# Optimization experiments

Measured on AMD Instinct MI355X. Metric: run time of the kernel, lower is better.

Reference implementation:

```python
import jax, jax.numpy as jnp
import numpy as np

B, S, D = 4, 2048, 2048
H, DH = 16, 128


def setup_inputs() -> dict:
    key = jax.random.key(0)
    k1, k2, k3, k4, k5 = jax.random.split(key, 5)
    x = jax.random.normal(k1, (B, S, D), dtype=jnp.float32)
    # causal mask, broadcast over heads and batch (module does mask.unsqueeze(0))
    attn_mask = jnp.tril(jnp.ones((S, S), dtype=jnp.int32))
    # torch Linear weights: [out, in]; scaled like default init
    w_qkv = jax.random.normal(k2, (3 * H * DH, D), dtype=jnp.float32) / np.sqrt(D)
    b_qkv = jax.random.normal(k3, (3 * H * DH,), dtype=jnp.float32) * 0.01
    w_out = jax.random.normal(k4, (D, H * DH), dtype=jnp.float32) / np.sqrt(H * DH)
    b_out = jax.random.normal(k5, (D,), dtype=jnp.float32) * 0.01
    return {"x": x, "attn_mask": attn_mask, "w_qkv": w_qkv, "b_qkv": b_qkv,
            "w_out": w_out, "b_out": b_out}


def reference(x, attn_mask, w_qkv, b_qkv, w_out, b_out):
    b, s, d = x.shape
    qkv = x @ w_qkv.T + b_qkv                      # [B,S,3*H*DH]
    qkv = qkv.reshape(b, s, H, 3 * DH)             # per-head contiguous 3*DH slice
    qkv = jnp.transpose(qkv, (2, 0, 1, 3))         # [H,B,S,3*DH]
    q, k, v = jnp.split(qkv, 3, axis=-1)           # each [H,B,S,DH]
    scores = jnp.einsum('hbqd,hbkd->hbqk', q, k) / np.sqrt(DH)
    scores = jnp.where(attn_mask[None, None] == 0, -jnp.inf, scores)
    attn = jax.nn.softmax(scores, axis=-1)         # dropout is identity at eval
    ctx = jnp.einsum('hbqk,hbkd->hbqd', attn, v)   # [H,B,S,DH]
    ctx = jnp.transpose(ctx, (1, 2, 0, 3)).reshape(b, s, H * DH)
    return ctx @ w_out.T + b_out
```

## Files before the change

### kernel.cpp

```cpp
#include <hip/hip_runtime.h>

typedef unsigned short u16;
typedef __bf16 bf16x8 __attribute__((ext_vector_type(8)));
typedef unsigned short u16x8 __attribute__((ext_vector_type(8)));
typedef float f32x4 __attribute__((ext_vector_type(4)));

#define GLDS16(gp, lp)                                                        \
  __builtin_amdgcn_global_load_lds(                                           \
      (const __attribute__((address_space(1))) void*)(gp),                    \
      (__attribute__((address_space(3))) void*)(lp), 16, 0, 0)

__device__ __forceinline__ u16 f2bf(float f) {
  unsigned u = __float_as_uint(f);
  u += 0x7FFFu + ((u >> 16) & 1u);
  return (u16)(u >> 16);
}

__device__ __forceinline__ f32x4 mfma_bf16(bf16x8 a, bf16x8 b, f32x4 c) {
  return __builtin_amdgcn_mfma_f32_16x16x32_bf16(a, b, c, 0, 0, 0);
}

__global__ void cvt_f32_bf16(const float* __restrict__ src,
                             u16* __restrict__ dst, int n8) {
  for (int i = blockIdx.x * blockDim.x + threadIdx.x; i < n8;
       i += gridDim.x * blockDim.x) {
    const float4* sp = (const float4*)src + (size_t)i * 2;
    float4 a = sp[0], b = sp[1];
    u16x8 o;
    o[0] = f2bf(a.x); o[1] = f2bf(a.y); o[2] = f2bf(a.z); o[3] = f2bf(a.w);
    o[4] = f2bf(b.x); o[5] = f2bf(b.y); o[6] = f2bf(b.z); o[7] = f2bf(b.w);
    *((u16x8*)dst + i) = o;
  }
}

template <int OUT_BF16>
__global__ __launch_bounds__(256) void gemm_bt(const u16* __restrict__ A,
                                               const u16* __restrict__ B,
                                               const float* __restrict__ bias,
                                               void* __restrict__ Cout, int M,
                                               int N, int K) {
  __shared__ __attribute__((aligned(16))) u16 As[128 * 64];
  __shared__ __attribute__((aligned(16))) u16 Bs[128 * 64];
  const int t = threadIdx.x, lane = t & 63, w = t >> 6;
  const int l15 = lane & 15, l4 = lane >> 4;
  const int bm = blockIdx.x * 128, bn = blockIdx.y * 128;
  const int wr = (w >> 1) * 64, wc = (w & 1) * 64;

  f32x4 z4 = {0.f, 0.f, 0.f, 0.f};
  f32x4 acc[4][4];
#pragma unroll
  for (int i = 0; i < 4; ++i)
#pragma unroll
    for (int j = 0; j < 4; ++j) acc[i][j] = z4;

  const int srow = t >> 3;
  const int scol = ((t & 7) ^ (srow & 7)) << 3;
  const u16* Ag = A + (size_t)(bm + srow) * K + scol;
  const u16* Bg = B + (size_t)(bn + srow) * K + scol;
  u16* AsW = As + w * 512;
  u16* BsW = Bs + w * 512;

  for (int k0 = 0; k0 < K; k0 += 64) {
    __syncthreads();
#pragma unroll
    for (int i = 0; i < 4; ++i) {
      GLDS16(Ag + k0 + i * 32 * K, AsW + i * 2048);
      GLDS16(Bg + k0 + i * 32 * K, BsW + i * 2048);
    }
    __syncthreads();
#pragma unroll
    for (int kc = 0; kc < 2; ++kc) {
      bf16x8 af[4], bf[4];
#pragma unroll
      for (int x = 0; x < 4; ++x) {
        int ra = wr + x * 16 + l15;
        af[x] = *(const bf16x8*)(As + ra * 64 + (((kc * 4 + l4) ^ (ra & 7)) << 3));
        int rb = wc + x * 16 + l15;
        bf[x] = *(const bf16x8*)(Bs + rb * 64 + (((kc * 4 + l4) ^ (rb & 7)) << 3));
      }
#pragma unroll
      for (int mi = 0; mi < 4; ++mi)
#pragma unroll
        for (int ni = 0; ni < 4; ++ni)
          acc[mi][ni] = mfma_bf16(af[mi], bf[ni], acc[mi][ni]);
    }
  }
  const int cr = l4 * 4, cc = l15;
#pragma unroll
  for (int ni = 0; ni < 4; ++ni) {
    int col = bn + wc + ni * 16 + cc;
    float bv = bias[col];
#pragma unroll
    for (int mi = 0; mi < 4; ++mi)
#pragma unroll
      for (int r = 0; r < 4; ++r) {
        int row = bm + wr + mi * 16 + cr + r;
        float v = acc[mi][ni][r] + bv;
        if (OUT_BF16)
          ((u16*)Cout)[(size_t)row * N + col] = f2bf(v);
        else
          ((float*)Cout)[(size_t)row * N + col] = v;
      }
  }
}

__device__ __forceinline__ int vt_idx(int d, int kk) {
  int swz = (d ^ (d >> 3)) & 7;
  return d * 64 + ((((kk >> 3) ^ swz) << 3) | (kk & 7));
}
__device__ __forceinline__ int ps_idx(int r, int c) {
  return r * 64 + ((((c >> 3) ^ ((r >> 2) & 7)) << 3) | (c & 7));
}

__global__ __launch_bounds__(256) void attn_fwd(const u16* __restrict__ qkv,
                                                u16* __restrict__ ctx) {
  constexpr int NQ = 6144, SD = 2048;
  __shared__ __attribute__((aligned(16))) u16 Ks[2][64 * 128];
  __shared__ __attribute__((aligned(16))) u16 Vt[2][128 * 64];
  __shared__ __attribute__((aligned(16))) u16 Ps[64 * 64];
  const int t = threadIdx.x, lane = t & 63, w = t >> 6;
  const int l15 = lane & 15, l4 = lane >> 4;
  const int h = blockIdx.y, b = blockIdx.z;
  const size_t rowbase = (size_t)b * SD;
  const int hq = h * 384;

  const u16* Kg = qkv + (rowbase + (t >> 4)) * NQ + hq + 128 +
                  (((t & 15) ^ ((t >> 4) & 7)) << 3);
  const u16* Vg = qkv + (rowbase + (t & 15)) * NQ + hq + 256 + ((t >> 4) << 3);
  const int vkk = t & 15, vd0 = (t >> 4) << 3;

  const float C = 0.12751879522447905f;
  const float THRC = 62.73592239488341f;

  for (int seg = 0; seg < 2; ++seg) {
    const int q0 = (seg == 0 ? (31 - (int)blockIdx.x) : (int)blockIdx.x) * 64;
    const int nt = (q0 >> 6) + 1;
    const int qrow = q0 + w * 16 + l4 * 4;

    bf16x8 qf[4];
    {
      const u16* qp = qkv + (rowbase + q0 + w * 16 + l15) * NQ + hq + l4 * 8;
#pragma unroll
      for (int kc = 0; kc < 4; ++kc) qf[kc] = *(const bf16x8*)(qp + kc * 32);
    }

    f32x4 z4 = {0.f, 0.f, 0.f, 0.f};
    f32x4 oacc[8];
#pragma unroll
    for (int i = 0; i < 8; ++i) oacc[i] = z4;
    float m_run[4], l_run[4];
#pragma unroll
    for (int r = 0; r < 4; ++r) { m_run[r] = -3.0e38f; l_run[r] = 0.f; }

    u16x8 vA[4], vB[4];
#pragma unroll
    for (int i = 0; i < 4; ++i)
      GLDS16(Kg + (size_t)(i * 16) * NQ, &Ks[0][i * 2048 + w * 512]);
#pragma unroll
    for (int p = 0; p < 4; ++p)
      vA[p] = *(const u16x8*)(Vg + (size_t)(p * 16) * NQ);
    __syncthreads();
#pragma unroll
    for (int p = 0; p < 4; ++p) {
      int kk = p * 16 + vkk;
#pragma unroll
      for (int j = 0; j < 8; ++j) Vt[0][vt_idx(vd0 + j, kk)] = vA[p][j];
    }
    {
      const int kv = (nt > 1) ? 64 : 0;
#pragma unroll
      for (int p = 0; p < 4; ++p)
        vA[p] = *(const u16x8*)(Vg + (size_t)(kv + p * 16) * NQ);
    }
    __syncthreads();

    for (int tt = 0; tt < nt; ++tt) {
      const int k0 = tt * 64, cur = tt & 1;
      const u16* KsC = &Ks[cur][0];
      u16* KsN = &Ks[cur ^ 1][0];
      const u16* VtC = &Vt[cur][0];
      u16* VtN = &Vt[cur ^ 1][0];

      const int kn = (k0 + 64 <= q0) ? k0 + 64 : q0;
#pragma unroll
      for (int i = 0; i < 4; ++i)
        GLDS16(Kg + (size_t)(kn + i * 16) * NQ, KsN + i * 2048 + w * 512);
      const int kv = (k0 + 128 <= q0) ? k0 + 128 : q0;
#pragma unroll
      for (int p = 0; p < 4; ++p)
        vB[p] = *(const u16x8*)(Vg + (size_t)(kv + p * 16) * NQ);

      f32x4 sc[4];
#pragma unroll
      for (int nf = 0; nf < 4; ++nf) sc[nf] = z4;
#pragma unroll
      for (int kc = 0; kc < 4; ++kc)
#pragma unroll
        for (int nf = 0; nf < 4; ++nf) {
          int rk = nf * 16 + l15;
          bf16x8 kf = *(const bf16x8*)(KsC + rk * 128 +
                                       (((kc * 4 + l4) ^ (rk & 7)) << 3));
          sc[nf] = mfma_bf16(qf[kc], kf, sc[nf]);
        }
      if (k0 == q0) {
#pragma unroll
        for (int nf = 0; nf < 4; ++nf) {
          int col = k0 + nf * 16 + l15;
#pragma unroll
          for (int r = 0; r < 4; ++r)
            if (col > qrow + r) sc[nf][r] = -3.0e38f;
        }
      }
      float mx[4];
#pragma unroll
      for (int r = 0; r < 4; ++r)
        mx[r] = fmaxf(fmaxf(sc[0][r], sc[1][r]), fmaxf(sc[2][r], sc[3][r]));
#pragma unroll
      for (int off = 8; off >= 1; off >>= 1)
#pragma unroll
        for (int r = 0; r < 4; ++r)
          mx[r] = fmaxf(mx[r], __shfl_xor(mx[r], off));
      bool upd = false;
#pragma unroll
      for (int r = 0; r < 4; ++r) upd |= (mx[r] > m_run[r] + THRC);
      if (__any(upd)) {
#pragma unroll
        for (int r = 0; r < 4; ++r) {
          float mn = fmaxf(m_run[r], mx[r]);
          float cr = exp2f((m_run[r] - mn) * C);
          m_run[r] = mn;
          l_run[r] *= cr;
#pragma unroll
          for (int nf = 0; nf < 8; ++nf) oacc[nf][r] *= cr;
        }
      }
      float mC[4], sm[4];
#pragma unroll
      for (int r = 0; r < 4; ++r) mC[r] = m_run[r] * C;
#pragma unroll
      for (int nf = 0; nf < 4; ++nf)
#pragma unroll
        for (int r = 0; r < 4; ++r)
          sc[nf][r] = exp2f(fmaf(sc[nf][r], C, -mC[r]));
#pragma unroll
      for (int r = 0; r < 4; ++r)
        sm[r] = (sc[0][r] + sc[1][r]) + (sc[2][r] + sc[3][r]);
#pragma unroll
      for (int off = 8; off >= 1; off >>= 1)
#pragma unroll
        for (int r = 0; r < 4; ++r) sm[r] += __shfl_xor(sm[r], off);
#pragma unroll
      for (int r = 0; r < 4; ++r) l_run[r] += sm[r];
#pragma unroll
      for (int nf = 0; nf < 4; ++nf)
#pragma unroll
        for (int r = 0; r < 4; ++r)
          ((__bf16*)Ps)[ps_idx(w * 16 + l4 * 4 + r, nf * 16 + l15)] =
              (__bf16)sc[nf][r];
#pragma unroll
      for (int p = 0; p < 4; ++p) {
        int kk = p * 16 + vkk;
#pragma unroll
        for (int j = 0; j < 8; ++j) VtN[vt_idx(vd0 + j, kk)] = vA[p][j];
      }
#pragma unroll
      for (int kc = 0; kc < 2; ++kc) {
        bf16x8 pf =
            *(const bf16x8*)(Ps + ps_idx(w * 16 + l15, kc * 32 + l4 * 8));
#pragma unroll
        for (int nf = 0; nf < 8; ++nf) {
          bf16x8 vf =
              *(const bf16x8*)(VtC + vt_idx(nf * 16 + l15, kc * 32 + l4 * 8));
          oacc[nf] = mfma_bf16(pf, vf, oacc[nf]);
        }
      }
      __syncthreads();
#pragma unroll
      for (int p = 0; p < 4; ++p) vA[p] = vB[p];
    }
    float inv[4];
#pragma unroll
    for (int r = 0; r < 4; ++r) inv[r] = 1.f / l_run[r];
    u16* cp = ctx + (rowbase + q0 + w * 16 + l4 * 4) * SD + h * 128 + l15;
#pragma unroll
    for (int nf = 0; nf < 8; ++nf)
#pragma unroll
      for (int r = 0; r < 4; ++r)
        ((__bf16*)cp)[(size_t)r * SD + nf * 16] =
            (__bf16)(oacc[nf][r] * inv[r]);
  }
}

extern "C" void kernel_launch(void* const* d_in, const int* in_sizes, int n_in,
                              void* d_out, int out_size, void* d_ws,
                              size_t ws_size, hipStream_t stream) {
  const float* x = (const float*)d_in[0];
  const float* wqkv = (const float*)d_in[2];
  const float* bqkv = (const float*)d_in[3];
  const float* wout = (const float*)d_in[4];
  const float* bout = (const float*)d_in[5];
  float* out = (float*)d_out;
  char* ws = (char*)d_ws;

  u16* xb = (u16*)(ws);
  u16* wqkvb = (u16*)(ws + 33554432);
  u16* woutb = (u16*)(ws + 58720256);
  u16* qkvb = (u16*)(ws + 67108864);
  u16* ctx = xb;

  cvt_f32_bf16<<<2048, 256, 0, stream>>>(x, xb, 16777216 / 8);
  cvt_f32_bf16<<<2048, 256, 0, stream>>>(wqkv, wqkvb, 12582912 / 8);
  cvt_f32_bf16<<<1024, 256, 0, stream>>>(wout, woutb, 4194304 / 8);
  gemm_bt<1><<<dim3(64, 48), 256, 0, stream>>>(xb, wqkvb, bqkv, qkvb, 8192,
                                               6144, 2048);
  attn_fwd<<<dim3(16, 16, 4), 256, 0, stream>>>(qkvb, ctx);
  gemm_bt<0><<<dim3(64, 16), 256, 0, stream>>>(ctx, woutb, bout, out, 8192,
                                               2048, 2048);
}
```

Before: 705.5 us.

## Enlarge attention query tile to 128 rows so each K/V tile is reused twice

The attention kernel now handles 128 query rows per block, two 16-row fragments per wave, instead of 64. Each K and V tile loaded into LDS therefore feeds twice as many MFMAs, which halves K/V global and LDS traffic per unit of work. The grid shrinks from 16 to 8 query-tile pairs and launch bounds request 2 blocks per CU. In exchange the kernel needs more accumulator registers and a larger Ps buffer, and the reduced block count may lower occupancy and worsen load balance.

```diff
diff --git a/kernel.cpp b/kernel.cpp
--- a/kernel.cpp
+++ b/kernel.cpp
@@ -112,16 +112,16 @@
   return r * 64 + ((((c >> 3) ^ ((r >> 2) & 7)) << 3) | (c & 7));
 }
 
-__global__ __launch_bounds__(256) void attn_fwd(const u16* __restrict__ qkv,
-                                                u16* __restrict__ ctx) {
+__global__ __launch_bounds__(256, 2) void attn_fwd(const u16* __restrict__ qkv,
+                                                   u16* __restrict__ ctx) {
   constexpr int NQ = 6144, SD = 2048;
   __shared__ __attribute__((aligned(16))) u16 Ks[2][64 * 128];
   __shared__ __attribute__((aligned(16))) u16 Vt[2][128 * 64];
-  __shared__ __attribute__((aligned(16))) u16 Ps[64 * 64];
+  __shared__ __attribute__((aligned(16))) u16 Ps[128 * 64];
   const int t = threadIdx.x, lane = t & 63, w = t >> 6;
   const int l15 = lane & 15, l4 = lane >> 4;
   const int h = blockIdx.y, b = blockIdx.z;
-  const size_t rowbase = (size_t)b * SD;
+  const size_t rowbase = (size_t)b * 2048;
   const int hq = h * 384;
 
   const u16* Kg = qkv + (rowbase + (t >> 4)) * NQ + hq + 128 +
@@ -133,24 +133,31 @@
   const float THRC = 62.73592239488341f;
 
   for (int seg = 0; seg < 2; ++seg) {
-    const int q0 = (seg == 0 ? (31 - (int)blockIdx.x) : (int)blockIdx.x) * 64;
-    const int nt = (q0 >> 6) + 1;
-    const int qrow = q0 + w * 16 + l4 * 4;
-
-    bf16x8 qf[4];
-    {
-      const u16* qp = qkv + (rowbase + q0 + w * 16 + l15) * NQ + hq + l4 * 8;
-#pragma unroll
-      for (int kc = 0; kc < 4; ++kc) qf[kc] = *(const bf16x8*)(qp + kc * 32);
+    const int qt = (seg == 0) ? (15 - (int)blockIdx.x) : (int)blockIdx.x;
+    const int q0 = qt * 128;
+    const int nt = 2 * qt + 2;
+    const int qr0 = q0 + w * 32 + l4 * 4;
+
+    bf16x8 qf[2][4];
+#pragma unroll
+    for (int mi = 0; mi < 2; ++mi) {
+      const u16* qp =
+          qkv + (rowbase + q0 + w * 32 + mi * 16 + l15) * NQ + hq + l4 * 8;
+#pragma unroll
+      for (int kc = 0; kc < 4; ++kc) qf[mi][kc] = *(const bf16x8*)(qp + kc * 32);
     }
 
     f32x4 z4 = {0.f, 0.f, 0.f, 0.f};
-    f32x4 oacc[8];
-#pragma unroll
-    for (int i = 0; i < 8; ++i) oacc[i] = z4;
-    float m_run[4], l_run[4];
-#pragma unroll
-    for (int r = 0; r < 4; ++r) { m_run[r] = -3.0e38f; l_run[r] = 0.f; }
+    f32x4 oacc[2][8];
+#pragma unroll
+    for (int mi = 0; mi < 2; ++mi)
+#pragma unroll
+      for (int i = 0; i < 8; ++i) oacc[mi][i] = z4;
+    float m_run[2][4], l_run[2][4];
+#pragma unroll
+    for (int mi = 0; mi < 2; ++mi)
+#pragma unroll
+      for (int r = 0; r < 4; ++r) { m_run[mi][r] = -3.0e38f; l_run[mi][r] = 0.f; }
 
     u16x8 vA[4], vB[4];
 #pragma unroll
@@ -166,128 +173,147 @@
 #pragma unroll
       for (int j = 0; j < 8; ++j) Vt[0][vt_idx(vd0 + j, kk)] = vA[p][j];
     }
-    {
-      const int kv = (nt > 1) ? 64 : 0;
-#pragma unroll
-      for (int p = 0; p < 4; ++p)
-        vA[p] = *(const u16x8*)(Vg + (size_t)(kv + p * 16) * NQ);
-    }
+#pragma unroll
+    for (int p = 0; p < 4; ++p)
+      vA[p] = *(const u16x8*)(Vg + (size_t)(64 + p * 16) * NQ);
     __syncthreads();
 
     for (int tt = 0; tt < nt; ++tt) {
       const int k0 = tt * 64, cur = tt & 1;
-      const u16* KsC = &Ks[cur][0];
-      u16* KsN = &Ks[cur ^ 1][0];
-      const u16* VtC = &Vt[cur][0];
-      u16* VtN = &Vt[cur ^ 1][0];
-
-      const int kn = (k0 + 64 <= q0) ? k0 + 64 : q0;
+      const int kn = (k0 + 64 < q0 + 64) ? k0 + 64 : q0 + 64;
 #pragma unroll
       for (int i = 0; i < 4; ++i)
-        GLDS16(Kg + (size_t)(kn + i * 16) * NQ, KsN + i * 2048 + w * 512);
-      const int kv = (k0 + 128 <= q0) ? k0 + 128 : q0;
+        GLDS16(Kg + (size_t)(kn + i * 16) * NQ,
+               &Ks[cur ^ 1][i * 2048 + w * 512]);
+      const int kv = (k0 + 128 < q0 + 64) ? k0 + 128 : q0 + 64;
 #pragma unroll
       for (int p = 0; p < 4; ++p)
         vB[p] = *(const u16x8*)(Vg + (size_t)(kv + p * 16) * NQ);
 
-      f32x4 sc[4];
-#pragma unroll
-      for (int nf = 0; nf < 4; ++nf) sc[nf] = z4;
+      f32x4 sc[2][4];
+#pragma unroll
+      for (int mi = 0; mi < 2; ++mi)
+#pragma unroll
+        for (int nf = 0; nf < 4; ++nf) sc[mi][nf] = z4;
 #pragma unroll
       for (int kc = 0; kc < 4; ++kc)
 #pragma unroll
         for (int nf = 0; nf < 4; ++nf) {
           int rk = nf * 16 + l15;
-          bf16x8 kf = *(const bf16x8*)(KsC + rk * 128 +
-                                       (((kc * 4 + l4) ^ (rk & 7)) << 3));
-          sc[nf] = mfma_bf16(qf[kc], kf, sc[nf]);
+          bf16x8 kf = *(const bf16x8*)(&Ks[cur][rk * 128 +
+                                              (((kc * 4 + l4) ^ (rk & 7)) << 3)]);
+          sc[0][nf] = mfma_bf16(qf[0][kc], kf, sc[0][nf]);
+          sc[1][nf] = mfma_bf16(qf[1][kc], kf, sc[1][nf]);
         }
-      if (k0 == q0) {
-#pragma unroll
-        for (int nf = 0; nf < 4; ++nf) {
-          int col = k0 + nf * 16 + l15;
+      if (tt + 2 >= nt) {
+#pragma unroll
+        for (int mi = 0; mi < 2; ++mi)
+#pragma unroll
+          for (int nf = 0; nf < 4; ++nf) {
+            int col = k0 + nf * 16 + l15;
+            int qr = qr0 + mi * 16;
+#pragma unroll
+            for (int r = 0; r < 4; ++r)
+              if (col > qr + r) sc[mi][nf][r] = -3.0e38f;
+          }
+      }
+      float mx[2][4];
+#pragma unroll
+      for (int mi = 0; mi < 2; ++mi)
+#pragma unroll
+        for (int r = 0; r < 4; ++r)
+          mx[mi][r] = fmaxf(fmaxf(sc[mi][0][r], sc[mi][1][r]),
+                            fmaxf(sc[mi][2][r], sc[mi][3][r]));
+#pragma unroll
+      for (int off = 8; off >= 1; off >>= 1)
+#pragma unroll
+        for (int mi = 0; mi < 2; ++mi)
 #pragma unroll
           for (int r = 0; r < 4; ++r)
-            if (col > qrow + r) sc[nf][r] = -3.0e38f;
-        }
-      }
-      float mx[4];
-#pragma unroll
-      for (int r = 0; r < 4; ++r)
-        mx[r] = fmaxf(fmaxf(sc[0][r], sc[1][r]), fmaxf(sc[2][r], sc[3][r]));
-#pragma unroll
-      for (int off = 8; off >= 1; off >>= 1)
+            mx[mi][r] = fmaxf(mx[mi][r], __shfl_xor(mx[mi][r], off));
+      bool upd = false;
+#pragma unroll
+      for (int mi = 0; mi < 2; ++mi)
 #pragma unroll
         for (int r = 0; r < 4; ++r)
-          mx[r] = fmaxf(mx[r], __shfl_xor(mx[r], off));
-      bool upd = false;
-#pragma unroll
-      for (int r = 0; r < 4; ++r) upd |= (mx[r] > m_run[r] + THRC);
+          upd |= (mx[mi][r] > m_run[mi][r] + THRC);
       if (__any(upd)) {
 #pragma unroll
-        for (int r = 0; r < 4; ++r) {
-          float mn = fmaxf(m_run[r], mx[r]);
-          float cr = exp2f((m_run[r] - mn) * C);
-          m_run[r] = mn;
-          l_run[r] *= cr;
-#pragma unroll
-          for (int nf = 0; nf < 8; ++nf) oacc[nf][r] *= cr;
-        }
-      }
-      float mC[4], sm[4];
-#pragma unroll
-      for (int r = 0; r < 4; ++r) mC[r] = m_run[r] * C;
-#pragma unroll
-      for (int nf = 0; nf < 4; ++nf)
+        for (int mi = 0; mi < 2; ++mi)
+#pragma unroll
+          for (int r = 0; r < 4; ++r) {
+            float mn = fmaxf(m_run[mi][r], mx[mi][r]);
+            float cr = exp2f((m_run[mi][r] - mn) * C);
+            m_run[mi][r] = mn;
+            l_run[mi][r] *= cr;
+#pragma unroll
+            for (int nf = 0; nf < 8; ++nf) oacc[mi][nf][r] *= cr;
+          }
+      }
+#pragma unroll
+      for (int mi = 0; mi < 2; ++mi) {
+        float mC[4], sm[4];
+#pragma unroll
+        for (int r = 0; r < 4; ++r) mC[r] = m_run[mi][r] * C;
+#pragma unroll
+        for (int nf = 0; nf < 4; ++nf)
+#pragma unroll
+          for (int r = 0; r < 4; ++r)
+            sc[mi][nf][r] = exp2f(fmaf(sc[mi][nf][r], C, -mC[r]));
 #pragma unroll
         for (int r = 0; r < 4; ++r)
-          sc[nf][r] = exp2f(fmaf(sc[nf][r], C, -mC[r]));
-#pragma unroll
-      for (int r = 0; r < 4; ++r)
-        sm[r] = (sc[0][r] + sc[1][r]) + (sc[2][r] + sc[3][r]);
-#pragma unroll
-      for (int off = 8; off >= 1; off >>= 1)
-#pragma unroll
-        for (int r = 0; r < 4; ++r) sm[r] += __shfl_xor(sm[r], off);
-#pragma unroll
-      for (int r = 0; r < 4; ++r) l_run[r] += sm[r];
-#pragma unroll
-      for (int nf = 0; nf < 4; ++nf)
-#pragma unroll
-        for (int r = 0; r < 4; ++r)
-          ((__bf16*)Ps)[ps_idx(w * 16 + l4 * 4 + r, nf * 16 + l15)] =
-              (__bf16)sc[nf][r];
+          sm[r] = (sc[mi][0][r] + sc[mi][1][r]) + (sc[mi][2][r] + sc[mi][3][r]);
+#pragma unroll
+        for (int off = 8; off >= 1; off >>= 1)
+#pragma unroll
+          for (int r = 0; r < 4; ++r) sm[r] += __shfl_xor(sm[r], off);
+#pragma unroll
+        for (int r = 0; r < 4; ++r) l_run[mi][r] += sm[r];
+#pragma unroll
+        for (int nf = 0; nf < 4; ++nf)
+#pragma unroll
+          for (int r = 0; r < 4; ++r)
+            ((__bf16*)Ps)[ps_idx(w * 32 + mi * 16 + l4 * 4 + r,
+                                 nf * 16 + l15)] = (__bf16)sc[mi][nf][r];
+      }
 #pragma unroll
       for (int p = 0; p < 4; ++p) {
         int kk = p * 16 + vkk;
 #pragma unroll
-        for (int j = 0; j < 8; ++j) VtN[vt_idx(vd0 + j, kk)] = vA[p][j];
+        for (int j = 0; j < 8; ++j) Vt[cur ^ 1][vt_idx(vd0 + j, kk)] = vA[p][j];
       }
 #pragma unroll
       for (int kc = 0; kc < 2; ++kc) {
-        bf16x8 pf =
-            *(const bf16x8*)(Ps + ps_idx(w * 16 + l15, kc * 32 + l4 * 8));
+        bf16x8 pf0 =
+            *(const bf16x8*)(Ps + ps_idx(w * 32 + l15, kc * 32 + l4 * 8));
+        bf16x8 pf1 =
+            *(const bf16x8*)(Ps + ps_idx(w * 32 + 16 + l15, kc * 32 + l4 * 8));
 #pragma unroll
         for (int nf = 0; nf < 8; ++nf) {
-          bf16x8 vf =
-              *(const bf16x8*)(VtC + vt_idx(nf * 16 + l15, kc * 32 + l4 * 8));
-          oacc[nf] = mfma_bf16(pf, vf, oacc[nf]);
+          bf16x8 vf = *(const bf16x8*)(&Vt[cur][vt_idx(nf * 16 + l15,
+                                                       kc * 32 + l4 * 8)]);
+          oacc[0][nf] = mfma_bf16(pf0, vf, oacc[0][nf]);
+          oacc[1][nf] = mfma_bf16(pf1, vf, oacc[1][nf]);
         }
       }
       __syncthreads();
 #pragma unroll
       for (int p = 0; p < 4; ++p) vA[p] = vB[p];
     }
-    float inv[4];
-#pragma unroll
-    for (int r = 0; r < 4; ++r) inv[r] = 1.f / l_run[r];
-    u16* cp = ctx + (rowbase + q0 + w * 16 + l4 * 4) * SD + h * 128 + l15;
-#pragma unroll
-    for (int nf = 0; nf < 8; ++nf)
-#pragma unroll
-      for (int r = 0; r < 4; ++r)
-        ((__bf16*)cp)[(size_t)r * SD + nf * 16] =
-            (__bf16)(oacc[nf][r] * inv[r]);
+#pragma unroll
+    for (int mi = 0; mi < 2; ++mi) {
+      float inv[4];
+#pragma unroll
+      for (int r = 0; r < 4; ++r) inv[r] = 1.f / l_run[mi][r];
+      u16* cp = ctx + (rowbase + q0 + w * 32 + mi * 16 + l4 * 4) * SD +
+                h * 128 + l15;
+#pragma unroll
+      for (int nf = 0; nf < 8; ++nf)
+#pragma unroll
+        for (int r = 0; r < 4; ++r)
+          ((__bf16*)cp)[(size_t)r * SD + nf * 16] =
+              (__bf16)(oacc[mi][nf][r] * inv[r]);
+    }
   }
 }
 
@@ -313,7 +339,7 @@
   cvt_f32_bf16<<<1024, 256, 0, stream>>>(wout, woutb, 4194304 / 8);
   gemm_bt<1><<<dim3(64, 48), 256, 0, stream>>>(xb, wqkvb, bqkv, qkvb, 8192,
                                                6144, 2048);
-  attn_fwd<<<dim3(16, 16, 4), 256, 0, stream>>>(qkvb, ctx);
+  attn_fwd<<<dim3(8, 16, 4), 256, 0, stream>>>(qkvb, ctx);
   gemm_bt<0><<<dim3(64, 16), 256, 0, stream>>>(ctx, woutb, bout, out, 8192,
                                                2048, 2048);
 }
```

Measured after the change: 688.4 us. -2.4%, faster.
